# Kernel optimization log

Hardware: AMD Instinct MI355X
Metric: run time of the kernel (lower is better)

Reference implementation:

```python
import jax, jax.numpy as jnp
import numpy as np

WS, WS2, UP = 8, 16, 2
DIM, HEADS = 192, 6
HD = DIM // HEADS
SCALE = HD ** -0.5
EPS = 1e-5

def _rel_index():
    r1, c1 = np.meshgrid(np.arange(WS), np.arange(WS), indexing='ij')
    r2, c2 = np.meshgrid(np.arange(WS2), np.arange(WS2), indexing='ij')
    r1, c1 = r1.ravel(), c1.ravel()          # 64 query positions
    r2, c2 = r2.ravel(), c2.ravel()          # 256 kv positions
    rel_row = r1[:, None] - r2[None, :]
    rel_col = c1[:, None] - c2[None, :]
    off = WS * UP - 1    # 15
    span = WS + WS * UP - 1  # 23
    return jnp.asarray((rel_row + off) * span + (rel_col + off))  # (64, 256)

REL_IDX = _rel_index()

def layer_norm(x, w, b):
    m = x.mean(-1, keepdims=True)
    v = ((x - m) ** 2).mean(-1, keepdims=True)
    return (x - m) * jax.lax.rsqrt(v + EPS) * w + b

def window_partition(x, ws):
    B, H, W, C = x.shape
    x = x.reshape(B, H // ws, ws, W // ws, ws, C).transpose(0, 1, 3, 2, 4, 5)
    return x.reshape(-1, ws * ws, C)

def window_reverse(w, ws, H, W, B):
    x = w.reshape(B, H // ws, W // ws, ws, ws, -1).transpose(0, 1, 3, 2, 4, 5)
    return x.reshape(B, H, W, -1)

def setup_inputs() -> dict:
    key = jax.random.key(0)
    ks = jax.random.split(key, 8)
    B, H, W, H2, W2 = 4, 128, 128, 256, 256
    s = 0.02
    return {
        'x': jax.random.normal(ks[0], (B, H * W, DIM), jnp.float32),
        'x2': jax.random.normal(ks[1], (B, H2 * W2, DIM), jnp.float32),
        'norm1_w': jnp.ones((DIM,), jnp.float32),
        'norm1_b': jnp.zeros((DIM,), jnp.float32),
        'qkv_w': jax.random.normal(ks[2], (DIM, DIM), jnp.float32) * s,
        'qkv_b': jnp.zeros((DIM,), jnp.float32),
        'qkv2_w': jax.random.normal(ks[3], (2 * DIM, DIM), jnp.float32) * s,
        'qkv2_b': jnp.zeros((2 * DIM,), jnp.float32),
        'rel_bias': jax.random.normal(ks[4], (23 * 23, HEADS), jnp.float32) * s,
        'proj_w': jax.random.normal(ks[5], (DIM, DIM), jnp.float32) * s,
        'proj_b': jnp.zeros((DIM,), jnp.float32),
        'norm2_w': jnp.ones((DIM,), jnp.float32),
        'norm2_b': jnp.zeros((DIM,), jnp.float32),
        'fc1_w': jax.random.normal(ks[6], (4 * DIM, DIM), jnp.float32) * s,
        'fc1_b': jnp.zeros((4 * DIM,), jnp.float32),
        'fc2_w': jax.random.normal(ks[7], (DIM, 4 * DIM), jnp.float32) * s,
        'fc2_b': jnp.zeros((DIM,), jnp.float32),
        'H': 128, 'W': 128, 'H2': 256, 'W2': 256,
    }

def reference(x, x2, norm1_w, norm1_b, qkv_w, qkv_b, qkv2_w, qkv2_b, rel_bias,
              proj_w, proj_b, norm2_w, norm2_b, fc1_w, fc1_b, fc2_w, fc2_b,
              H, W, H2, W2):
    B, L, C = x.shape
    shortcut = x
    xn = layer_norm(x, norm1_w, norm1_b).reshape(B, H, W, C)
    x2r = x2.reshape(B, H2, W2, C)

    xw = window_partition(xn, WS)      # (nW, 64, C)
    x2w = window_partition(x2r, WS2)   # (nW, 256, C)

    q = (xw @ qkv_w.T + qkv_b).reshape(-1, WS * WS, HEADS, HD).transpose(0, 2, 1, 3)
    kv = (x2w @ qkv2_w.T + qkv2_b).reshape(-1, WS2 * WS2, 2, HEADS, HD).transpose(2, 0, 3, 1, 4)
    k, v = kv[0], kv[1]                # (nW, h, 256, d)

    attn = jnp.einsum('whnd,whmd->whnm', q * SCALE, k)   # (nW, h, 64, 256)
    bias = rel_bias[REL_IDX]                             # (64, 256, h)
    attn = attn + bias.transpose(2, 0, 1)[None]
    attn = jax.nn.softmax(attn, axis=-1)
    out = jnp.einsum('whnm,whmd->wnhd', attn, v).reshape(-1, WS * WS, C)
    out = out @ proj_w.T + proj_b

    x = shortcut + window_reverse(out, WS, H, W, B).reshape(B, H * W, C)
    h = layer_norm(x, norm2_w, norm2_b)
    h = jax.nn.gelu(h @ fc1_w.T + fc1_b, approximate=False)
    x = x + (h @ fc2_w.T + fc2_b)
    return x
```

## Files before the change

kernel.cpp:

```cpp
#include <hip/hip_runtime.h>
#include <hip/hip_bf16.h>
#include <math.h>

typedef unsigned int u32;
typedef unsigned short u16;

typedef __attribute__((ext_vector_type(8))) short bf16x8;
typedef __attribute__((ext_vector_type(4))) float f32x4;

__device__ __forceinline__ float bflo(u32 u){ union{u32 i; float f;} c; c.i = u << 16; return c.f; }
__device__ __forceinline__ float bfhi(u32 u){ union{u32 i; float f;} c; c.i = u & 0xffff0000u; return c.f; }
__device__ __forceinline__ float bfs(u16 s){ union{u32 i; float f;} c; c.i = ((u32)s) << 16; return c.f; }
__device__ __forceinline__ u32 packbf(float a, float b){
  union{float f; u32 i;} ca, cb; ca.f = a; cb.f = b;
  u32 ua = (ca.i + 0x7fffu + ((ca.i >> 16) & 1u)) >> 16;
  u32 ub = (cb.i + 0x7fffu + ((cb.i >> 16) & 1u)) >> 16;
  return (ua & 0xffffu) | (ub << 16);
}
__device__ __forceinline__ u16 bf1(float a){
  union{float f; u32 i;} c; c.f = a;
  return (u16)((c.i + 0x7fffu + ((c.i >> 16) & 1u)) >> 16);
}
__device__ __forceinline__ bf16x8 pack8(float f0,float f1,float f2,float f3,
                                        float f4,float f5,float f6,float f7){
  union { u32 u[4]; bf16x8 v; } cv;
  cv.u[0]=packbf(f0,f1); cv.u[1]=packbf(f2,f3); cv.u[2]=packbf(f4,f5); cv.u[3]=packbf(f6,f7);
  return cv.v;
}
__device__ __forceinline__ float gelu_exact(float v){ return 0.5f*v*(1.0f + erff(v*0.70710678118654752f)); }
__device__ __forceinline__ bool detect_f32(const u32* rawn1){ return (rawn1[0] & 0xFFFFu) == 0u; }

#define SCALE_Q 0.17677669529663687f

#define P_N1W 0
#define P_N1B 192
#define P_N2W 384
#define P_N2B 576
#define P_QKVB 768
#define P_QKV2B 960
#define P_PROJB 1344
#define P_FC1B 1536
#define P_FC2B 2304
#define P_RELB 2496
#define P_TOTAL 5670
#define W_QKV 0
#define W_QKV2 18432
#define W_PROJ 55296
#define W_FC1 73728
#define W_FC2 147456
#define W_TOTAL 221184

__device__ __forceinline__ void stage_w64x192(const u32* __restrict__ src, u32* lds, int tid){
  #pragma unroll
  for (int t = 0; t < 6; ++t) {
    int idx = tid + t*256;
    int j = idx / 24, seg = idx % 24;
    uint4 v = *(const uint4*)(src + (size_t)j*96 + seg*4);
    int byt = (j*384 + seg*16) ^ ((j&7)<<4);
    *(uint4*)((char*)lds + byt) = v;
  }
}
__device__ __forceinline__ bf16x8 lds_w64(const u32* lds, int j, int kt, int g){
  int byt = (j*384 + kt*64 + g*16) ^ ((j&7)<<4);
  return *(const bf16x8*)((const char*)lds + byt);
}
__device__ __forceinline__ bf16x8 lds_w192(const u32* lds, int j, int kk, int g){
  int byt = (j*128 + kk*64 + g*16) ^ ((j&7)<<4);
  return *(const bf16x8*)((const char*)lds + byt);
}

typedef __attribute__((address_space(1))) const u32 gas_u32c;
typedef __attribute__((address_space(3))) u32 las_u32;
__device__ __forceinline__ void gld_lds16(const u32* g, u32* l){
  gas_u32c* gp = (gas_u32c*)(unsigned long long)(size_t)g;
  las_u32*  lp = (las_u32*)(unsigned int)(size_t)l;
  __builtin_amdgcn_global_load_lds(gp, lp, 16, 0, 0);
}
__device__ __forceinline__ void issue_w64x192(const u32* src, u32* lds, int w, int l){
  #pragma unroll
  for (int t = 0; t < 3; ++t) {
    int seg = w + t*8;
    int a = seg*1024 + l*16;
    int j = a / 384;
    int off = a - j*384;
    const u32* g = src + (size_t)j*96 + ((off ^ ((j&7)<<4)) >> 2);
    gld_lds16(g, lds + seg*256);
  }
}
__device__ __forceinline__ void issue_w32x192_t512(const u32* src, u32* lds, int w, int l){
  {
    int seg = w;
    int a = seg*1024 + l*16;
    int j = a / 384;
    int off = a - j*384;
    const u32* g = src + (size_t)j*96 + ((off ^ ((j&7)<<4)) >> 2);
    gld_lds16(g, lds + seg*256);
  }
  if (w < 4) {
    int seg = w + 8;
    int a = seg*1024 + l*16;
    int j = a / 384;
    int off = a - j*384;
    const u32* g = src + (size_t)j*96 + ((off ^ ((j&7)<<4)) >> 2);
    gld_lds16(g, lds + seg*256);
  }
}
__device__ __forceinline__ void issue_w192x64(const u32* src, int ch, u32* lds, int w, int l){
  #pragma unroll
  for (int t = 0; t < 3; ++t) {
    int seg = w + t*8;
    int a = seg*1024 + l*16;
    int j = a >> 7;
    int off = a & 127;
    const u32* g = src + (size_t)j*384 + ch*32 + ((off ^ ((j&7)<<4)) >> 2);
    gld_lds16(g, lds + seg*256);
  }
}

__global__ __launch_bounds__(256) void k_canon_w(
    const void* qkvw, const void* qkv2w, const void* projw,
    const void* fc1w, const void* fc2w, const u32* rawn1, u32* cw)
{
  int idx = blockIdx.x*256 + threadIdx.x;
  bool isf32 = detect_f32(rawn1);
  const void* src; int off;
  if      (idx < W_QKV2){ src=qkvw;  off=idx; }
  else if (idx < W_PROJ){ src=qkv2w; off=idx-W_QKV2; }
  else if (idx < W_FC1) { src=projw; off=idx-W_PROJ; }
  else if (idx < W_FC2) { src=fc1w;  off=idx-W_FC1; }
  else                  { src=fc2w;  off=idx-W_FC2; }
  u32 o;
  if (isf32) { float2 v = ((const float2*)src)[off]; o = packbf(v.x, v.y); }
  else       { o = ((const u32*)src)[off]; }
  cw[idx] = o;
}

__global__ __launch_bounds__(256) void k_canon_v(
    const void* n1w, const void* n1b, const void* n2w, const void* n2b,
    const void* qkvb, const void* qkv2b, const void* projb,
    const void* fc1b, const void* fc2b, const void* relb,
    const u32* rawn1, float* par)
{
  int idx = blockIdx.x*256 + threadIdx.x;
  if (idx >= P_TOTAL) return;
  bool isf32 = detect_f32(rawn1);
  const void* src; int off;
  if      (idx < P_N1B)  { src=n1w;  off=idx; }
  else if (idx < P_N2W)  { src=n1b;  off=idx-P_N1B; }
  else if (idx < P_N2B)  { src=n2w;  off=idx-P_N2W; }
  else if (idx < P_QKVB) { src=n2b;  off=idx-P_N2B; }
  else if (idx < P_QKV2B){ src=qkvb; off=idx-P_QKVB; }
  else if (idx < P_PROJB){ src=qkv2b;off=idx-P_QKV2B; }
  else if (idx < P_FC1B) { src=projb;off=idx-P_PROJB; }
  else if (idx < P_FC2B) { src=fc1b; off=idx-P_FC1B; }
  else if (idx < P_RELB) { src=fc2b; off=idx-P_FC2B; }
  else                   { src=relb; off=idx-P_RELB; }
  par[idx] = isf32 ? ((const float*)src)[off] : bfs(((const u16*)src)[off]);
}

__global__ __launch_bounds__(256) void k_bias(
    const float* __restrict__ par, float* __restrict__ tbl)
{
  int idx = blockIdx.x*256 + threadIdx.x;
  int h  = idx >> 12;
  int remi = idx & 4095;
  int kt = remi >> 8;
  int qt = (remi >> 6) & 3;
  int ll = idx & 63;
  int lr = ll & 15, g = ll >> 4;
  int q = qt*16 + lr;
  int r1 = q >> 3, c1 = q & 7;
  float vv[4];
  #pragma unroll
  for (int i = 0; i < 4; ++i) {
    int kv = kt*16 + 4*g + i;
    int r2 = kv >> 4, c2 = kv & 15;
    vv[i] = par[P_RELB + ((r1-r2+15)*23 + (c1-c2+15))*6 + h];
  }
  ((float4*)tbl)[idx] = make_float4(vv[0], vv[1], vv[2], vv[3]);
}

__global__ __launch_bounds__(256) void k_qproj(
    const void* __restrict__ x, const u32* __restrict__ rawn1,
    const u32* __restrict__ cw, const float* __restrict__ par,
    u16* __restrict__ q_ws)
{
  __shared__ u32 wbuf[6144];
  int tid = threadIdx.x;
  int l = tid & 63, w = tid >> 6, lr = l & 15, g = l >> 4;
  int wi = blockIdx.x;
  int b = wi >> 8, rem = wi & 255, wh = rem >> 4, ww = rem & 15;
  bool isf32 = detect_f32(rawn1);

  bf16x8 a[6];
  {
    int t = w*16 + lr;
    int r = t >> 3, c = t & 7;
    size_t grow = (size_t)b*16384 + (size_t)(wh*8+r)*128 + (ww*8+c);
    float4 xf[12];
    if (isf32) {
      const float* xp = (const float*)x + grow*192;
      #pragma unroll
      for (int kt = 0; kt < 6; ++kt) {
        xf[kt*2]   = *(const float4*)(xp + kt*32 + 8*g);
        xf[kt*2+1] = *(const float4*)(xp + kt*32 + 8*g + 4);
      }
    } else {
      const u32* xp = (const u32*)x + grow*96;
      #pragma unroll
      for (int kt = 0; kt < 6; ++kt) {
        uint4 u = *(const uint4*)(xp + kt*16 + 4*g);
        xf[kt*2]   = make_float4(bflo(u.x), bfhi(u.x), bflo(u.y), bfhi(u.y));
        xf[kt*2+1] = make_float4(bflo(u.z), bfhi(u.z), bflo(u.w), bfhi(u.w));
      }
    }
    float s = 0.f, s2 = 0.f;
    #pragma unroll
    for (int q8 = 0; q8 < 12; ++q8) {
      s  += xf[q8].x + xf[q8].y + xf[q8].z + xf[q8].w;
      s2 += xf[q8].x*xf[q8].x + xf[q8].y*xf[q8].y + xf[q8].z*xf[q8].z + xf[q8].w*xf[q8].w;
    }
    s += __shfl_xor(s, 16); s2 += __shfl_xor(s2, 16);
    s += __shfl_xor(s, 32); s2 += __shfl_xor(s2, 32);
    float m = s * (1.f/192.f);
    float rstd = rsqrtf(s2*(1.f/192.f) - m*m + 1e-5f);
    #pragma unroll
    for (int kt = 0; kt < 6; ++kt) {
      int k0 = kt*32 + 8*g;
      float4 w0 = *(const float4*)(par + P_N1W + k0);
      float4 w1 = *(const float4*)(par + P_N1W + k0 + 4);
      float4 b0 = *(const float4*)(par + P_N1B + k0);
      float4 b1 = *(const float4*)(par + P_N1B + k0 + 4);
      float4 f0 = xf[kt*2], f1 = xf[kt*2+1];
      a[kt] = pack8((f0.x-m)*rstd*w0.x + b0.x, (f0.y-m)*rstd*w0.y + b0.y,
                    (f0.z-m)*rstd*w0.z + b0.z, (f0.w-m)*rstd*w0.w + b0.w,
                    (f1.x-m)*rstd*w1.x + b1.x, (f1.y-m)*rstd*w1.y + b1.y,
                    (f1.z-m)*rstd*w1.z + b1.z, (f1.w-m)*rstd*w1.w + b1.w);
    }
  }

  for (int ch = 0; ch < 3; ++ch) {
    __syncthreads();
    stage_w64x192(cw + W_QKV + (size_t)(ch*64)*96, wbuf, tid);
    __syncthreads();
    #pragma unroll
    for (int nt2 = 0; nt2 < 4; ++nt2) {
      int j = ch*64 + nt2*16 + lr;
      f32x4 acc = {0.f,0.f,0.f,0.f};
      #pragma unroll
      for (int kt = 0; kt < 6; ++kt) {
        bf16x8 bb = lds_w64(wbuf, nt2*16 + lr, kt, g);
        acc = __builtin_amdgcn_mfma_f32_16x16x32_bf16(a[kt], bb, acc, 0, 0, 0);
      }
      float bj = par[P_QKVB + j];
      int h = j >> 5, d = j & 31;
      #pragma unroll
      for (int i = 0; i < 4; ++i) {
        int n = w*16 + 4*g + i;
        q_ws[(size_t)(wi*6+h)*2048 + (size_t)n*32 + d] = bf1((acc[i] + bj) * SCALE_Q);
      }
    }
  }
}

__global__ __launch_bounds__(512) void k_kvproj(
    const void* __restrict__ x2, const u32* __restrict__ rawn1,
    const u32* __restrict__ cw, const float* __restrict__ par,
    u16* __restrict__ k_ws, u16* __restrict__ v_ws, int win0)
{
  __shared__ u32 wbufA[3072];
  __shared__ u32 wbufB[3072];
  __shared__ u16 ot[12288];
  int tid = threadIdx.x;
  int l = tid & 63, w = tid >> 6, lr = l & 15, g = l >> 4;
  int lwi = blockIdx.x;
  int wi = win0 + lwi;
  int b = wi >> 8, rem = wi & 255, wh = rem >> 4, ww = rem & 15;
  bool isf32 = detect_f32(rawn1);

  issue_w32x192_t512(cw + W_QKV2, wbufA, w, l);

  bf16x8 a[2][6];
  #pragma unroll
  for (int mt = 0; mt < 2; ++mt) {
    int tt = w*32 + mt*16 + lr;
    int r = tt >> 4, c = tt & 15;
    size_t grow = (size_t)b*65536 + (size_t)(wh*16+r)*256 + (ww*16+c);
    if (isf32) {
      const float4* xp = (const float4*)x2 + grow*48;
      #pragma unroll
      for (int kt = 0; kt < 6; ++kt) {
        float4 f0 = xp[kt*8 + g*2];
        float4 f1 = xp[kt*8 + g*2 + 1];
        a[mt][kt] = pack8(f0.x,f0.y,f0.z,f0.w, f1.x,f1.y,f1.z,f1.w);
      }
    } else {
      const u32* xp = (const u32*)x2 + grow*96;
      #pragma unroll
      for (int kt = 0; kt < 6; ++kt)
        a[mt][kt] = *(const bf16x8*)(xp + kt*16 + g*4);
    }
  }
  __syncthreads();

  for (int c = 0; c < 12; ++c) {
    const u32* buf = (c & 1) ? wbufB : wbufA;
    u32* nxt = (c & 1) ? wbufA : wbufB;
    if (c < 11)
      issue_w32x192_t512(cw + W_QKV2 + (size_t)((c+1)*32)*96, nxt, w, l);
    if (c < 6) {
      #pragma unroll
      for (int mt = 0; mt < 2; ++mt)
        #pragma unroll
        for (int nt2 = 0; nt2 < 2; ++nt2) {
          int jl = nt2*16 + lr;
          f32x4 acc = {0.f,0.f,0.f,0.f};
          #pragma unroll
          for (int kt = 0; kt < 6; ++kt) {
            bf16x8 bb = lds_w64(buf, jl, kt, g);
            acc = __builtin_amdgcn_mfma_f32_16x16x32_bf16(a[mt][kt], bb, acc, 0, 0, 0);
          }
          float bj = par[P_QKV2B + c*32 + jl];
          #pragma unroll
          for (int i = 0; i < 4; ++i)
            ot[(w*32 + mt*16 + 4*g + i)*48 + jl] = bf1(acc[i] + bj);
        }
      __syncthreads();
      #pragma unroll
      for (int t = 0; t < 2; ++t) {
        int u = tid + t*512;
        int tok = u >> 2, dseg = u & 3;
        uint4 v = *(const uint4*)&ot[tok*48 + dseg*8];
        *(uint4*)(k_ws + (size_t)(lwi*6 + c)*8192 + (size_t)tok*32 + dseg*8) = v;
      }
    } else {
      int nv = c - 6;
      #pragma unroll
      for (int mt = 0; mt < 2; ++mt)
        #pragma unroll
        for (int nt2 = 0; nt2 < 2; ++nt2) {
          f32x4 acc = {0.f,0.f,0.f,0.f};
          #pragma unroll
          for (int kt = 0; kt < 6; ++kt) {
            bf16x8 bb = lds_w64(buf, nt2*16 + lr, kt, g);
            acc = __builtin_amdgcn_mfma_f32_16x16x32_bf16(bb, a[mt][kt], acc, 0, 0, 0);
          }
          int jl0 = nt2*16 + 4*g;
          #pragma unroll
          for (int i = 0; i < 4; ++i)
            ot[(jl0 + i)*264 + w*32 + mt*16 + lr] = bf1(acc[i] + par[P_QKV2B + 192 + nv*32 + jl0 + i]);
        }
      __syncthreads();
      #pragma unroll
      for (int t = 0; t < 2; ++t) {
        int u = tid + t*512;
        int jrow = u >> 5, seg = u & 31;
        uint4 v = *(const uint4*)&ot[jrow*264 + seg*8];
        *(uint4*)(v_ws + (size_t)(lwi*6 + nv)*8192 + (size_t)jrow*256 + seg*8) = v;
      }
    }
    __syncthreads();
  }
}

__global__ __launch_bounds__(256) void k_attn(
    const u16* __restrict__ q_ws, const u16* __restrict__ k_ws,
    const u16* __restrict__ v_ws, const float* __restrict__ tbl,
    u16* __restrict__ O_ws, int win0)
{
  __shared__ u32 Psh[4*1024];
  __shared__ float msh[2][2][4];
  int tid = threadIdx.x;
  int w = tid >> 6, l = tid & 63;
  int lr = l & 15, g = l >> 4;
  int pairi = w >> 1, half = w & 1;
  int task = blockIdx.x*2 + pairi;
  int lwi = task / 6, h = task - lwi*6;
  int wi = win0 + lwi;

  bf16x8 qb[4];
  {
    const u16* qp = q_ws + (size_t)(wi*6+h)*2048;
    #pragma unroll
    for (int qt = 0; qt < 4; ++qt)
      qb[qt] = *(const bf16x8*)(qp + (qt*16 + lr)*32 + 8*g);
  }
  const u16* kp = k_ws + (size_t)(lwi*6+h)*8192;
  const u16* vp = v_ws + (size_t)(lwi*6+h)*8192;
  const float4* tb4 = (const float4*)tbl + (size_t)h*4096 + l;

  f32x4 ao[2][4];
  #pragma unroll
  for (int dt = 0; dt < 2; ++dt)
    #pragma unroll
    for (int qt = 0; qt < 4; ++qt) ao[dt][qt] = (f32x4){0.f,0.f,0.f,0.f};
  float mreg[4] = {-3.0e38f,-3.0e38f,-3.0e38f,-3.0e38f};
  float sreg[4] = {0.f,0.f,0.f,0.f};
  u32* pbu = Psh + w*1024;

  for (int ch = half*4; ch < half*4 + 4; ++ch) {
    bf16x8 ka0 = *(const bf16x8*)(kp + (2*ch)*512   + lr*32 + 8*g);
    bf16x8 ka1 = *(const bf16x8*)(kp + (2*ch+1)*512 + lr*32 + 8*g);
    f32x4 s0[4], s1[4];
    #pragma unroll
    for (int qt = 0; qt < 4; ++qt) {
      float4 b0 = tb4[(2*ch)*256   + qt*64];
      float4 b1 = tb4[(2*ch+1)*256 + qt*64];
      f32x4 c0; c0[0]=b0.x; c0[1]=b0.y; c0[2]=b0.z; c0[3]=b0.w;
      f32x4 c1; c1[0]=b1.x; c1[1]=b1.y; c1[2]=b1.z; c1[3]=b1.w;
      s0[qt] = __builtin_amdgcn_mfma_f32_16x16x32_bf16(ka0, qb[qt], c0, 0, 0, 0);
      s1[qt] = __builtin_amdgcn_mfma_f32_16x16x32_bf16(ka1, qb[qt], c1, 0, 0, 0);
    }
    #pragma unroll
    for (int qt = 0; qt < 4; ++qt) {
      float pm = fmaxf(fmaxf(fmaxf(s0[qt][0],s0[qt][1]), fmaxf(s0[qt][2],s0[qt][3])),
                       fmaxf(fmaxf(s1[qt][0],s1[qt][1]), fmaxf(s1[qt][2],s1[qt][3])));
      pm = fmaxf(pm, __shfl_xor(pm, 16));
      pm = fmaxf(pm, __shfl_xor(pm, 32));
      if (!__all(pm - mreg[qt] <= 8.0f)) {
        float nm = fmaxf(mreg[qt], pm);
        float resc = __expf(mreg[qt] - nm);
        mreg[qt] = nm;
        sreg[qt] *= resc;
        #pragma unroll
        for (int dt = 0; dt < 2; ++dt) {
          ao[dt][qt][0] *= resc; ao[dt][qt][1] *= resc;
          ao[dt][qt][2] *= resc; ao[dt][qt][3] *= resc;
        }
      }
      float nm = mreg[qt];
      float p00 = __expf(s0[qt][0]-nm), p01 = __expf(s0[qt][1]-nm),
            p02 = __expf(s0[qt][2]-nm), p03 = __expf(s0[qt][3]-nm);
      float p10 = __expf(s1[qt][0]-nm), p11 = __expf(s1[qt][1]-nm),
            p12 = __expf(s1[qt][2]-nm), p13 = __expf(s1[qt][3]-nm);
      float ps = ((p00+p01)+(p02+p03)) + ((p10+p11)+(p12+p13));
      ps += __shfl_xor(ps, 16);
      ps += __shfl_xor(ps, 32);
      sreg[qt] += ps;
      int row = qt*16 + lr;
      int sw = (row & 3) << 2;
      *(uint2*)&pbu[row*16 + ((2*g) ^ sw)]     = make_uint2(packbf(p00,p01), packbf(p02,p03));
      *(uint2*)&pbu[row*16 + ((8 + 2*g) ^ sw)] = make_uint2(packbf(p10,p11), packbf(p12,p13));
    }
    asm volatile("" ::: "memory");
    bf16x8 va0 = *(const bf16x8*)(vp + lr*256        + ch*32 + 8*g);
    bf16x8 va1 = *(const bf16x8*)(vp + (16 + lr)*256 + ch*32 + 8*g);
    #pragma unroll
    for (int qt = 0; qt < 4; ++qt) {
      int row = qt*16 + lr;
      int sw = (row & 3) << 2;
      bf16x8 pa = *(const bf16x8*)&pbu[row*16 + ((4*g) ^ sw)];
      ao[0][qt] = __builtin_amdgcn_mfma_f32_16x16x32_bf16(va0, pa, ao[0][qt], 0, 0, 0);
      ao[1][qt] = __builtin_amdgcn_mfma_f32_16x16x32_bf16(va1, pa, ao[1][qt], 0, 0, 0);
    }
    asm volatile("" ::: "memory");
  }

  __syncthreads();
  if (half == 1) {
    float* dst = (float*)(Psh + pairi*2048);
    #pragma unroll
    for (int dt = 0; dt < 2; ++dt)
      #pragma unroll
      for (int qt = 0; qt < 4; ++qt)
        #pragma unroll
        for (int i = 0; i < 4; ++i)
          dst[(dt*16 + qt*4 + i)*64 + l] = ao[dt][qt][i];
    if (l == 0) {
      msh[pairi][0][0] = mreg[0]; msh[pairi][0][1] = mreg[1];
      msh[pairi][0][2] = mreg[2]; msh[pairi][0][3] = mreg[3];
      msh[pairi][1][0] = sreg[0]; msh[pairi][1][1] = sreg[1];
      msh[pairi][1][2] = sreg[2]; msh[pairi][1][3] = sreg[3];
    }
  }
  __syncthreads();
  if (half == 0) {
    const float* src = (const float*)(Psh + pairi*2048);
    #pragma unroll
    for (int qt = 0; qt < 4; ++qt) {
      float m1 = msh[pairi][0][qt], s1 = msh[pairi][1][qt];
      float M = fmaxf(mreg[qt], m1);
      float e0 = __expf(mreg[qt] - M), e1 = __expf(m1 - M);
      float rs = 1.0f / (sreg[qt]*e0 + s1*e1);
      u16* orow = O_ws + ((size_t)(wi*64) + qt*16 + lr)*192 + h*32;
      #pragma unroll
      for (int dt = 0; dt < 2; ++dt)
        #pragma unroll
        for (int i = 0; i < 4; ++i) {
          float o = ao[dt][qt][i]*e0 + src[(dt*16 + qt*4 + i)*64 + l]*e1;
          orow[dt*16 + 4*g + i] = bf1(o * rs);
        }
    }
  }
}

__global__ __launch_bounds__(256) void k_proj(
    const u16* __restrict__ O_ws, const u32* __restrict__ cw,
    const float* __restrict__ par, const void* __restrict__ x,
    const u32* __restrict__ rawn1, float* __restrict__ xres)
{
  __shared__ u32 wbuf[6144];
  int wi = blockIdx.x;
  int b = wi >> 8, rem = wi & 255, wh = rem >> 4, ww = rem & 15;
  int tid = threadIdx.x;
  int l = tid & 63, w = tid >> 6, lr = l & 15, g = l >> 4;
  bool isf32 = detect_f32(rawn1);
  int t = w*16 + lr;
  const u16* op = O_ws + (size_t)(wi*64 + t)*192;
  bf16x8 a[6];
  #pragma unroll
  for (int kt = 0; kt < 6; ++kt) a[kt] = *(const bf16x8*)(op + kt*32 + 8*g);

  for (int ch = 0; ch < 3; ++ch) {
    __syncthreads();
    stage_w64x192(cw + W_PROJ + (size_t)(ch*64)*96, wbuf, tid);
    __syncthreads();
    #pragma unroll
    for (int nt2 = 0; nt2 < 4; ++nt2) {
      int j = ch*64 + nt2*16 + lr;
      f32x4 acc = {0.f,0.f,0.f,0.f};
      #pragma unroll
      for (int kt = 0; kt < 6; ++kt) {
        bf16x8 bb = lds_w64(wbuf, nt2*16 + lr, kt, g);
        acc = __builtin_amdgcn_mfma_f32_16x16x32_bf16(a[kt], bb, acc, 0, 0, 0);
      }
      float bj = par[P_PROJB + j];
      #pragma unroll
      for (int i = 0; i < 4; ++i) {
        int tok = w*16 + 4*g + i;
        int rr = tok >> 3, cc = tok & 7;
        size_t grow = (size_t)b*16384 + (size_t)(wh*8+rr)*128 + (ww*8+cc);
        float sres = isf32 ? ((const float*)x)[grow*192 + j]
                           : bfs(((const u16*)x)[grow*192 + j]);
        xres[grow*192 + j] = sres + acc[i] + bj;
      }
    }
  }
}

__global__ __launch_bounds__(512) void k_mlp(
    const float* __restrict__ xres, const u32* __restrict__ cw,
    const float* __restrict__ par, float* __restrict__ out)
{
  __shared__ u32 wbufA[6144];
  __shared__ u32 wbufB[6144];
  __shared__ u16 Hc[8][32][64];
  int tid = threadIdx.x;
  int l = tid & 63, w = tid >> 6;
  int lr = l & 15, g = l >> 4;
  size_t row0 = (size_t)blockIdx.x * 256;

  bf16x8 a[2][6];
  #pragma unroll
  for (int mt = 0; mt < 2; ++mt) {
    size_t t = row0 + w*32 + mt*16 + lr;
    const float* xr = xres + t*192;
    float4 xf[12];
    #pragma unroll
    for (int kt = 0; kt < 6; ++kt) {
      xf[kt*2]   = *(const float4*)(xr + kt*32 + 8*g);
      xf[kt*2+1] = *(const float4*)(xr + kt*32 + 8*g + 4);
    }
    float s = 0.f, s2 = 0.f;
    #pragma unroll
    for (int q = 0; q < 12; ++q) {
      s  += xf[q].x + xf[q].y + xf[q].z + xf[q].w;
      s2 += xf[q].x*xf[q].x + xf[q].y*xf[q].y + xf[q].z*xf[q].z + xf[q].w*xf[q].w;
    }
    s += __shfl_xor(s, 16); s2 += __shfl_xor(s2, 16);
    s += __shfl_xor(s, 32); s2 += __shfl_xor(s2, 32);
    float m = s * (1.f/192.f);
    float rstd = rsqrtf(s2*(1.f/192.f) - m*m + 1e-5f);
    #pragma unroll
    for (int kt = 0; kt < 6; ++kt) {
      int k0 = kt*32 + 8*g;
      float4 w0 = *(const float4*)(par + P_N2W + k0);
      float4 w1 = *(const float4*)(par + P_N2W + k0 + 4);
      float4 b0 = *(const float4*)(par + P_N2B + k0);
      float4 b1 = *(const float4*)(par + P_N2B + k0 + 4);
      float4 f0 = xf[kt*2], f1 = xf[kt*2+1];
      a[mt][kt] = pack8((f0.x-m)*rstd*w0.x + b0.x, (f0.y-m)*rstd*w0.y + b0.y,
                        (f0.z-m)*rstd*w0.z + b0.z, (f0.w-m)*rstd*w0.w + b0.w,
                        (f1.x-m)*rstd*w1.x + b1.x, (f1.y-m)*rstd*w1.y + b1.y,
                        (f1.z-m)*rstd*w1.z + b1.z, (f1.w-m)*rstd*w1.w + b1.w);
    }
  }

  f32x4 acc2[2][12];
  #pragma unroll
  for (int mt = 0; mt < 2; ++mt)
    #pragma unroll
    for (int i = 0; i < 12; ++i) acc2[mt][i] = (f32x4){0.f,0.f,0.f,0.f};

  char* hbase = (char*)&Hc[w][0][0];
  const u32* w1p = cw + W_FC1;
  const u32* w2p = cw + W_FC2;

  issue_w64x192(w1p, wbufA, w, l);
  __syncthreads();

  for (int ch = 0; ch < 12; ++ch) {
    issue_w192x64(w2p, ch, wbufB, w, l);
    #pragma unroll
    for (int nt2 = 0; nt2 < 4; ++nt2) {
      f32x4 acc0 = {0.f,0.f,0.f,0.f}, acc1 = {0.f,0.f,0.f,0.f};
      #pragma unroll
      for (int kt = 0; kt < 6; ++kt) {
        bf16x8 bb = lds_w64(wbufA, nt2*16 + lr, kt, g);
        acc0 = __builtin_amdgcn_mfma_f32_16x16x32_bf16(a[0][kt], bb, acc0, 0, 0, 0);
        acc1 = __builtin_amdgcn_mfma_f32_16x16x32_bf16(a[1][kt], bb, acc1, 0, 0, 0);
      }
      float bj = par[P_FC1B + ch*64 + nt2*16 + lr];
      #pragma unroll
      for (int mt = 0; mt < 2; ++mt) {
        f32x4 acc = mt ? acc1 : acc0;
        #pragma unroll
        for (int i = 0; i < 4; ++i) {
          int row = mt*16 + 4*g + i;
          int byt = (row*128 + (nt2*16+lr)*2) ^ ((row&7)<<4);
          *(u16*)(hbase + byt) = bf1(gelu_exact(acc[i] + bj));
        }
      }
    }
    __syncthreads();
    if (ch < 11) issue_w64x192(w1p + (size_t)((ch+1)*64)*96, wbufA, w, l);
    #pragma unroll
    for (int kk = 0; kk < 2; ++kk) {
      bf16x8 a20, a21;
      {
        int row0h = lr, row1h = 16 + lr;
        a20 = *(const bf16x8*)(hbase + ((row0h*128 + kk*64 + g*16) ^ ((row0h&7)<<4)));
        a21 = *(const bf16x8*)(hbase + ((row1h*128 + kk*64 + g*16) ^ ((row1h&7)<<4)));
      }
      #pragma unroll
      for (int nt = 0; nt < 12; ++nt) {
        bf16x8 bb = lds_w192(wbufB, nt*16 + lr, kk, g);
        acc2[0][nt] = __builtin_amdgcn_mfma_f32_16x16x32_bf16(a20, bb, acc2[0][nt], 0, 0, 0);
        acc2[1][nt] = __builtin_amdgcn_mfma_f32_16x16x32_bf16(a21, bb, acc2[1][nt], 0, 0, 0);
      }
    }
    __syncthreads();
  }

  #pragma unroll
  for (int mt = 0; mt < 2; ++mt) {
    size_t trow = row0 + w*32 + mt*16 + 4*g;
    #pragma unroll
    for (int nt = 0; nt < 12; ++nt) {
      int j = nt*16 + lr;
      float bj = par[P_FC2B + j];
      #pragma unroll
      for (int i = 0; i < 4; ++i)
        out[(trow+i)*192 + j] = xres[(trow+i)*192 + j] + acc2[mt][nt][i] + bj;
    }
  }
}

extern "C" void kernel_launch(void* const* d_in, const int* in_sizes, int n_in,
                              void* d_out, int out_size, void* d_ws, size_t ws_size,
                              hipStream_t stream) {
  const void* x      = d_in[0];
  const void* x2     = d_in[1];
  const void* n1w    = d_in[2];
  const void* n1b    = d_in[3];
  const void* qkv_w  = d_in[4];
  const void* qkv_b  = d_in[5];
  const void* qkv2_w = d_in[6];
  const void* qkv2_b = d_in[7];
  const void* relb   = d_in[8];
  const void* proj_w = d_in[9];
  const void* proj_b = d_in[10];
  const void* n2w    = d_in[11];
  const void* n2b    = d_in[12];
  const void* fc1_w  = d_in[13];
  const void* fc1_b  = d_in[14];
  const void* fc2_w  = d_in[15];
  const void* fc2_b  = d_in[16];
  const u32* rawn1   = (const u32*)d_in[2];
  float* out = (float*)d_out;

  int nslice = (ws_size >= 303290520ull) ? 1 : (ws_size >= 202700000ull) ? 2 : 4;
  int nw = 1024 / nslice;
  size_t kvb = (size_t)nw * 98304;

  char* ws = (char*)d_ws;
  u16*   q_ws = (u16*)ws;
  u16*   k_ws = (u16*)(ws + 25165824);
  u16*   v_ws = (u16*)(ws + 25165824 + kvb);
  u16*   O_ws = (u16*)(ws + 25165824 + 2*kvb);
  float* xres = (float*)(ws + 50331648 + 2*kvb);
  u32*   cw   = (u32*)(ws + 100663296 + 2*kvb);
  float* tbl  = (float*)(ws + 100663296 + 2*kvb + 884736);
  float* par  = (float*)(ws + 100663296 + 2*kvb + 884736 + 393216);

  k_canon_w<<<W_TOTAL/256, 256, 0, stream>>>(qkv_w, qkv2_w, proj_w, fc1_w, fc2_w, rawn1, cw);
  k_canon_v<<<(P_TOTAL+255)/256, 256, 0, stream>>>(n1w, n1b, n2w, n2b, qkv_b, qkv2_b,
                                                   proj_b, fc1_b, fc2_b, relb, rawn1, par);
  k_bias  <<<96, 256, 0, stream>>>(par, tbl);
  k_qproj <<<1024, 256, 0, stream>>>(x, rawn1, cw, par, q_ws);
  for (int s = 0; s < nslice; ++s) {
    int win0 = s*nw;
    k_kvproj<<<nw,   512, 0, stream>>>(x2, rawn1, cw, par, k_ws, v_ws, win0);
    k_attn  <<<nw*3, 256, 0, stream>>>(q_ws, k_ws, v_ws, tbl, O_ws, win0);
  }
  k_proj  <<<1024, 256, 0, stream>>>(O_ws, cw, par, x, rawn1, xres);
  k_mlp   <<< 256, 512, 0, stream>>>(xres, cw, par, out);
}
```

Baseline: 631.5 us.

## Fuse KV projection with window attention, keeping K/V in shared memory

Merges the KV projection kernel and the attention kernel into one kernel per window. Each head's K and V are computed into swizzled LDS tiles and consumed immediately, so the K/V round trip through global memory and the sliced launch loop are gone. Attention is now split across 8 waves, one per 32-key chunk, each doing a single-chunk softmax. Partial results are merged through LDS with a cross-wave max/sum reduction. The cost is heavy LDS use (about 110KB, likely one block per CU) and three block-wide barriers per head.

```diff
diff --git a/kernel.cpp b/kernel.cpp
--- a/kernel.cpp
+++ b/kernel.cpp
@@ -263,22 +263,25 @@
   }
 }
 
-__global__ __launch_bounds__(512) void k_kvproj(
+__global__ __launch_bounds__(512) void k_kvattn(
     const void* __restrict__ x2, const u32* __restrict__ rawn1,
     const u32* __restrict__ cw, const float* __restrict__ par,
-    u16* __restrict__ k_ws, u16* __restrict__ v_ws, int win0)
+    const u16* __restrict__ q_ws, const float* __restrict__ tbl,
+    u16* __restrict__ O_ws, int win0)
 {
-  __shared__ u32 wbufA[3072];
-  __shared__ u32 wbufB[3072];
-  __shared__ u16 ot[12288];
+  __shared__ u32 wK[3072];
+  __shared__ u32 wV[3072];
+  __shared__ u16 Ksh[8192];
+  __shared__ u16 Vsh[8192];
+  __shared__ float un[17920];
   int tid = threadIdx.x;
   int l = tid & 63, w = tid >> 6, lr = l & 15, g = l >> 4;
-  int lwi = blockIdx.x;
-  int wi = win0 + lwi;
+  int wi = win0 + blockIdx.x;
   int b = wi >> 8, rem = wi & 255, wh = rem >> 4, ww = rem & 15;
   bool isf32 = detect_f32(rawn1);
 
-  issue_w32x192_t512(cw + W_QKV2, wbufA, w, l);
+  issue_w32x192_t512(cw + W_QKV2, wK, w, l);
+  issue_w32x192_t512(cw + W_QKV2 + (size_t)192*96, wV, w, l);
 
   bf16x8 a[2][6];
   #pragma unroll
@@ -303,148 +306,102 @@
   }
   __syncthreads();
 
-  for (int c = 0; c < 12; ++c) {
-    const u32* buf = (c & 1) ? wbufB : wbufA;
-    u32* nxt = (c & 1) ? wbufA : wbufB;
-    if (c < 11)
-      issue_w32x192_t512(cw + W_QKV2 + (size_t)((c+1)*32)*96, nxt, w, l);
-    if (c < 6) {
-      #pragma unroll
-      for (int mt = 0; mt < 2; ++mt)
+  for (int h = 0; h < 6; ++h) {
+    #pragma unroll
+    for (int mt = 0; mt < 2; ++mt)
+      #pragma unroll
+      for (int nt2 = 0; nt2 < 2; ++nt2) {
+        int jl = nt2*16 + lr;
+        f32x4 acc = {0.f,0.f,0.f,0.f};
         #pragma unroll
-        for (int nt2 = 0; nt2 < 2; ++nt2) {
-          int jl = nt2*16 + lr;
-          f32x4 acc = {0.f,0.f,0.f,0.f};
-          #pragma unroll
-          for (int kt = 0; kt < 6; ++kt) {
-            bf16x8 bb = lds_w64(buf, jl, kt, g);
-            acc = __builtin_amdgcn_mfma_f32_16x16x32_bf16(a[mt][kt], bb, acc, 0, 0, 0);
-          }
-          float bj = par[P_QKV2B + c*32 + jl];
-          #pragma unroll
-          for (int i = 0; i < 4; ++i)
-            ot[(w*32 + mt*16 + 4*g + i)*48 + jl] = bf1(acc[i] + bj);
+        for (int kt = 0; kt < 6; ++kt) {
+          bf16x8 bb = lds_w64(wK, jl, kt, g);
+          acc = __builtin_amdgcn_mfma_f32_16x16x32_bf16(a[mt][kt], bb, acc, 0, 0, 0);
         }
-      __syncthreads();
-      #pragma unroll
-      for (int t = 0; t < 2; ++t) {
-        int u = tid + t*512;
-        int tok = u >> 2, dseg = u & 3;
-        uint4 v = *(const uint4*)&ot[tok*48 + dseg*8];
-        *(uint4*)(k_ws + (size_t)(lwi*6 + c)*8192 + (size_t)tok*32 + dseg*8) = v;
-      }
-    } else {
-      int nv = c - 6;
-      #pragma unroll
-      for (int mt = 0; mt < 2; ++mt)
+        float bj = par[P_QKV2B + h*32 + jl];
         #pragma unroll
-        for (int nt2 = 0; nt2 < 2; ++nt2) {
-          f32x4 acc = {0.f,0.f,0.f,0.f};
-          #pragma unroll
-          for (int kt = 0; kt < 6; ++kt) {
-            bf16x8 bb = lds_w64(buf, nt2*16 + lr, kt, g);
-            acc = __builtin_amdgcn_mfma_f32_16x16x32_bf16(bb, a[mt][kt], acc, 0, 0, 0);
-          }
-          int jl0 = nt2*16 + 4*g;
-          #pragma unroll
-          for (int i = 0; i < 4; ++i)
-            ot[(jl0 + i)*264 + w*32 + mt*16 + lr] = bf1(acc[i] + par[P_QKV2B + 192 + nv*32 + jl0 + i]);
+        for (int i = 0; i < 4; ++i) {
+          int tok = w*32 + mt*16 + 4*g + i;
+          *(u16*)((char*)Ksh + tok*64 + ((jl*2) ^ ((tok&3)<<4))) = bf1(acc[i] + bj);
         }
-      __syncthreads();
-      #pragma unroll
-      for (int t = 0; t < 2; ++t) {
-        int u = tid + t*512;
-        int jrow = u >> 5, seg = u & 31;
-        uint4 v = *(const uint4*)&ot[jrow*264 + seg*8];
-        *(uint4*)(v_ws + (size_t)(lwi*6 + nv)*8192 + (size_t)jrow*256 + seg*8) = v;
-      }
-    }
-    __syncthreads();
-  }
-}
-
-__global__ __launch_bounds__(256) void k_attn(
-    const u16* __restrict__ q_ws, const u16* __restrict__ k_ws,
-    const u16* __restrict__ v_ws, const float* __restrict__ tbl,
-    u16* __restrict__ O_ws, int win0)
-{
-  __shared__ u32 Psh[4*1024];
-  __shared__ float msh[2][2][4];
-  int tid = threadIdx.x;
-  int w = tid >> 6, l = tid & 63;
-  int lr = l & 15, g = l >> 4;
-  int pairi = w >> 1, half = w & 1;
-  int task = blockIdx.x*2 + pairi;
-  int lwi = task / 6, h = task - lwi*6;
-  int wi = win0 + lwi;
-
-  bf16x8 qb[4];
-  {
-    const u16* qp = q_ws + (size_t)(wi*6+h)*2048;
-    #pragma unroll
-    for (int qt = 0; qt < 4; ++qt)
-      qb[qt] = *(const bf16x8*)(qp + (qt*16 + lr)*32 + 8*g);
-  }
-  const u16* kp = k_ws + (size_t)(lwi*6+h)*8192;
-  const u16* vp = v_ws + (size_t)(lwi*6+h)*8192;
-  const float4* tb4 = (const float4*)tbl + (size_t)h*4096 + l;
-
-  f32x4 ao[2][4];
-  #pragma unroll
-  for (int dt = 0; dt < 2; ++dt)
-    #pragma unroll
-    for (int qt = 0; qt < 4; ++qt) ao[dt][qt] = (f32x4){0.f,0.f,0.f,0.f};
-  float mreg[4] = {-3.0e38f,-3.0e38f,-3.0e38f,-3.0e38f};
-  float sreg[4] = {0.f,0.f,0.f,0.f};
-  u32* pbu = Psh + w*1024;
-
-  for (int ch = half*4; ch < half*4 + 4; ++ch) {
-    bf16x8 ka0 = *(const bf16x8*)(kp + (2*ch)*512   + lr*32 + 8*g);
-    bf16x8 ka1 = *(const bf16x8*)(kp + (2*ch+1)*512 + lr*32 + 8*g);
+      }
+    #pragma unroll
+    for (int mt = 0; mt < 2; ++mt)
+      #pragma unroll
+      for (int nt2 = 0; nt2 < 2; ++nt2) {
+        f32x4 acc = {0.f,0.f,0.f,0.f};
+        #pragma unroll
+        for (int kt = 0; kt < 6; ++kt) {
+          bf16x8 bb = lds_w64(wV, nt2*16 + lr, kt, g);
+          acc = __builtin_amdgcn_mfma_f32_16x16x32_bf16(bb, a[mt][kt], acc, 0, 0, 0);
+        }
+        int jl0 = nt2*16 + 4*g;
+        int tok = w*32 + mt*16 + lr;
+        #pragma unroll
+        for (int i = 0; i < 4; ++i) {
+          int jr = jl0 + i;
+          *(u16*)((char*)Vsh + jr*512 + ((tok*2) ^ ((jr&7)<<4)))
+            = bf1(acc[i] + par[P_QKV2B + 192 + h*32 + jr]);
+        }
+      }
+    __syncthreads();
+    if (h < 5) {
+      issue_w32x192_t512(cw + W_QKV2 + (size_t)((h+1)*32)*96, wK, w, l);
+      issue_w32x192_t512(cw + W_QKV2 + (size_t)(192 + (h+1)*32)*96, wV, w, l);
+    }
+
+    bf16x8 qb[4];
+    {
+      const u16* qp = q_ws + (size_t)(wi*6+h)*2048;
+      #pragma unroll
+      for (int qt = 0; qt < 4; ++qt)
+        qb[qt] = *(const bf16x8*)(qp + (qt*16 + lr)*32 + 8*g);
+    }
+    const float4* tb4 = (const float4*)tbl + (size_t)h*4096 + l;
+    int t0 = w*32 + lr, t1 = w*32 + 16 + lr;
+    bf16x8 ka0 = *(const bf16x8*)((const char*)Ksh + t0*64 + ((g*16) ^ ((t0&3)<<4)));
+    bf16x8 ka1 = *(const bf16x8*)((const char*)Ksh + t1*64 + ((g*16) ^ ((t1&3)<<4)));
     f32x4 s0[4], s1[4];
     #pragma unroll
     for (int qt = 0; qt < 4; ++qt) {
-      float4 b0 = tb4[(2*ch)*256   + qt*64];
-      float4 b1 = tb4[(2*ch+1)*256 + qt*64];
+      float4 b0 = tb4[(2*w)*256   + qt*64];
+      float4 b1 = tb4[(2*w+1)*256 + qt*64];
       f32x4 c0; c0[0]=b0.x; c0[1]=b0.y; c0[2]=b0.z; c0[3]=b0.w;
       f32x4 c1; c1[0]=b1.x; c1[1]=b1.y; c1[2]=b1.z; c1[3]=b1.w;
       s0[qt] = __builtin_amdgcn_mfma_f32_16x16x32_bf16(ka0, qb[qt], c0, 0, 0, 0);
       s1[qt] = __builtin_amdgcn_mfma_f32_16x16x32_bf16(ka1, qb[qt], c1, 0, 0, 0);
     }
+    u32* pbu = (u32*)un + w*1024;
+    float mv[4], sv[4];
+    f32x4 ao[2][4];
+    #pragma unroll
+    for (int dt = 0; dt < 2; ++dt)
+      #pragma unroll
+      for (int qt = 0; qt < 4; ++qt) ao[dt][qt] = (f32x4){0.f,0.f,0.f,0.f};
     #pragma unroll
     for (int qt = 0; qt < 4; ++qt) {
       float pm = fmaxf(fmaxf(fmaxf(s0[qt][0],s0[qt][1]), fmaxf(s0[qt][2],s0[qt][3])),
                        fmaxf(fmaxf(s1[qt][0],s1[qt][1]), fmaxf(s1[qt][2],s1[qt][3])));
       pm = fmaxf(pm, __shfl_xor(pm, 16));
       pm = fmaxf(pm, __shfl_xor(pm, 32));
-      if (!__all(pm - mreg[qt] <= 8.0f)) {
-        float nm = fmaxf(mreg[qt], pm);
-        float resc = __expf(mreg[qt] - nm);
-        mreg[qt] = nm;
-        sreg[qt] *= resc;
-        #pragma unroll
-        for (int dt = 0; dt < 2; ++dt) {
-          ao[dt][qt][0] *= resc; ao[dt][qt][1] *= resc;
-          ao[dt][qt][2] *= resc; ao[dt][qt][3] *= resc;
-        }
-      }
-      float nm = mreg[qt];
-      float p00 = __expf(s0[qt][0]-nm), p01 = __expf(s0[qt][1]-nm),
-            p02 = __expf(s0[qt][2]-nm), p03 = __expf(s0[qt][3]-nm);
-      float p10 = __expf(s1[qt][0]-nm), p11 = __expf(s1[qt][1]-nm),
-            p12 = __expf(s1[qt][2]-nm), p13 = __expf(s1[qt][3]-nm);
+      float p00 = __expf(s0[qt][0]-pm), p01 = __expf(s0[qt][1]-pm),
+            p02 = __expf(s0[qt][2]-pm), p03 = __expf(s0[qt][3]-pm);
+      float p10 = __expf(s1[qt][0]-pm), p11 = __expf(s1[qt][1]-pm),
+            p12 = __expf(s1[qt][2]-pm), p13 = __expf(s1[qt][3]-pm);
       float ps = ((p00+p01)+(p02+p03)) + ((p10+p11)+(p12+p13));
       ps += __shfl_xor(ps, 16);
       ps += __shfl_xor(ps, 32);
-      sreg[qt] += ps;
+      mv[qt] = pm; sv[qt] = ps;
       int row = qt*16 + lr;
       int sw = (row & 3) << 2;
       *(uint2*)&pbu[row*16 + ((2*g) ^ sw)]     = make_uint2(packbf(p00,p01), packbf(p02,p03));
       *(uint2*)&pbu[row*16 + ((8 + 2*g) ^ sw)] = make_uint2(packbf(p10,p11), packbf(p12,p13));
     }
     asm volatile("" ::: "memory");
-    bf16x8 va0 = *(const bf16x8*)(vp + lr*256        + ch*32 + 8*g);
-    bf16x8 va1 = *(const bf16x8*)(vp + (16 + lr)*256 + ch*32 + 8*g);
+    bf16x8 va0 = *(const bf16x8*)((const char*)Vsh + lr*512
+                    + (((w*32 + 8*g)*2) ^ ((lr&7)<<4)));
+    bf16x8 va1 = *(const bf16x8*)((const char*)Vsh + (16+lr)*512
+                    + (((w*32 + 8*g)*2) ^ ((lr&7)<<4)));
     #pragma unroll
     for (int qt = 0; qt < 4; ++qt) {
       int row = qt*16 + lr;
@@ -453,44 +410,42 @@
       ao[0][qt] = __builtin_amdgcn_mfma_f32_16x16x32_bf16(va0, pa, ao[0][qt], 0, 0, 0);
       ao[1][qt] = __builtin_amdgcn_mfma_f32_16x16x32_bf16(va1, pa, ao[1][qt], 0, 0, 0);
     }
-    asm volatile("" ::: "memory");
-  }
-
-  __syncthreads();
-  if (half == 1) {
-    float* dst = (float*)(Psh + pairi*2048);
-    #pragma unroll
-    for (int dt = 0; dt < 2; ++dt)
-      #pragma unroll
-      for (int qt = 0; qt < 4; ++qt)
+    __syncthreads();
+
+    #pragma unroll
+    for (int qt = 0; qt < 4; ++qt) {
+      int q = qt*16 + lr;
+      #pragma unroll
+      for (int dt = 0; dt < 2; ++dt)
         #pragma unroll
         for (int i = 0; i < 4; ++i)
-          dst[(dt*16 + qt*4 + i)*64 + l] = ao[dt][qt][i];
-    if (l == 0) {
-      msh[pairi][0][0] = mreg[0]; msh[pairi][0][1] = mreg[1];
-      msh[pairi][0][2] = mreg[2]; msh[pairi][0][3] = mreg[3];
-      msh[pairi][1][0] = sreg[0]; msh[pairi][1][1] = sreg[1];
-      msh[pairi][1][2] = sreg[2]; msh[pairi][1][3] = sreg[3];
-    }
-  }
-  __syncthreads();
-  if (half == 0) {
-    const float* src = (const float*)(Psh + pairi*2048);
-    #pragma unroll
-    for (int qt = 0; qt < 4; ++qt) {
-      float m1 = msh[pairi][0][qt], s1 = msh[pairi][1][qt];
-      float M = fmaxf(mreg[qt], m1);
-      float e0 = __expf(mreg[qt] - M), e1 = __expf(m1 - M);
-      float rs = 1.0f / (sreg[qt]*e0 + s1*e1);
-      u16* orow = O_ws + ((size_t)(wi*64) + qt*16 + lr)*192 + h*32;
-      #pragma unroll
-      for (int dt = 0; dt < 2; ++dt)
-        #pragma unroll
-        for (int i = 0; i < 4; ++i) {
-          float o = ao[dt][qt][i]*e0 + src[(dt*16 + qt*4 + i)*64 + l]*e1;
-          orow[dt*16 + 4*g + i] = bf1(o * rs);
-        }
-    }
+          un[w*2112 + q*33 + dt*16 + 4*g + i] = ao[dt][qt][i];
+      if (g == 0) {
+        un[16896 + w*64 + q] = mv[qt];
+        un[17408 + w*64 + q] = sv[qt];
+      }
+    }
+    __syncthreads();
+
+    {
+      int q = tid >> 3, db = (tid & 7)*4;
+      float M = -3.0e38f;
+      #pragma unroll
+      for (int w8 = 0; w8 < 8; ++w8) M = fmaxf(M, un[16896 + w8*64 + q]);
+      float S = 0.f, o0 = 0.f, o1 = 0.f, o2 = 0.f, o3 = 0.f;
+      #pragma unroll
+      for (int w8 = 0; w8 < 8; ++w8) {
+        float e = __expf(un[16896 + w8*64 + q] - M);
+        S += un[17408 + w8*64 + q] * e;
+        const float* ob = un + w8*2112 + q*33 + db;
+        o0 += ob[0]*e; o1 += ob[1]*e; o2 += ob[2]*e; o3 += ob[3]*e;
+      }
+      float rs = 1.0f / S;
+      u16* orow = O_ws + ((size_t)(wi*64) + q)*192 + h*32 + db;
+      orow[0] = bf1(o0*rs); orow[1] = bf1(o1*rs);
+      orow[2] = bf1(o2*rs); orow[3] = bf1(o3*rs);
+    }
+    __syncthreads();
   }
 }
 
@@ -679,30 +634,20 @@
   const u32* rawn1   = (const u32*)d_in[2];
   float* out = (float*)d_out;
 
-  int nslice = (ws_size >= 303290520ull) ? 1 : (ws_size >= 202700000ull) ? 2 : 4;
-  int nw = 1024 / nslice;
-  size_t kvb = (size_t)nw * 98304;
-
   char* ws = (char*)d_ws;
   u16*   q_ws = (u16*)ws;
-  u16*   k_ws = (u16*)(ws + 25165824);
-  u16*   v_ws = (u16*)(ws + 25165824 + kvb);
-  u16*   O_ws = (u16*)(ws + 25165824 + 2*kvb);
-  float* xres = (float*)(ws + 50331648 + 2*kvb);
-  u32*   cw   = (u32*)(ws + 100663296 + 2*kvb);
-  float* tbl  = (float*)(ws + 100663296 + 2*kvb + 884736);
-  float* par  = (float*)(ws + 100663296 + 2*kvb + 884736 + 393216);
+  u16*   O_ws = (u16*)(ws + 25165824);
+  float* xres = (float*)(ws + 50331648);
+  u32*   cw   = (u32*)(ws + 100663296);
+  float* tbl  = (float*)(ws + 100663296 + 884736);
+  float* par  = (float*)(ws + 100663296 + 884736 + 393216);
 
   k_canon_w<<<W_TOTAL/256, 256, 0, stream>>>(qkv_w, qkv2_w, proj_w, fc1_w, fc2_w, rawn1, cw);
   k_canon_v<<<(P_TOTAL+255)/256, 256, 0, stream>>>(n1w, n1b, n2w, n2b, qkv_b, qkv2_b,
                                                    proj_b, fc1_b, fc2_b, relb, rawn1, par);
   k_bias  <<<96, 256, 0, stream>>>(par, tbl);
   k_qproj <<<1024, 256, 0, stream>>>(x, rawn1, cw, par, q_ws);
-  for (int s = 0; s < nslice; ++s) {
-    int win0 = s*nw;
-    k_kvproj<<<nw,   512, 0, stream>>>(x2, rawn1, cw, par, k_ws, v_ws, win0);
-    k_attn  <<<nw*3, 256, 0, stream>>>(q_ws, k_ws, v_ws, tbl, O_ws, win0);
-  }
+  k_kvattn<<<1024, 512, 0, stream>>>(x2, rawn1, cw, par, q_ws, tbl, O_ws, 0);
   k_proj  <<<1024, 256, 0, stream>>>(O_ws, cw, par, x, rawn1, xres);
   k_mlp   <<< 256, 512, 0, stream>>>(xres, cw, par, out);
 }
```

Measured after the change: 639.6 us. Within noise of the previous version (+1.3%).
